# Kernel optimization log

Measured on AMD Instinct MI355X. Metric: run time of the kernel, lower is better.

## Reference

```python
import jax, jax.numpy as jnp
import numpy as np

H = 32        # num query heads
KVH = 8       # num kv heads
HD = 64       # head dim
G = H // KVH  # GQA group size
THETA = 10000.0


def _rope(x, pos):
    # x: [B, h, S, HD], pos: [B, S] int
    inv_freq = 1.0 / (THETA ** (jnp.arange(0, HD, 2, dtype=jnp.float32) / HD))  # [HD/2]
    freqs = pos.astype(jnp.float32)[:, :, None] * inv_freq[None, None, :]        # [B, S, HD/2]
    emb = jnp.concatenate([freqs, freqs], axis=-1)                               # [B, S, HD]
    cos = jnp.cos(emb)[:, None, :, :].astype(x.dtype)                            # [B, 1, S, HD]
    sin = jnp.sin(emb)[:, None, :, :].astype(x.dtype)
    x1, x2 = x[..., : HD // 2], x[..., HD // 2 :]
    rot = jnp.concatenate([-x2, x1], axis=-1)
    return x * cos + rot * sin


def setup_inputs() -> dict:
    key = jax.random.key(0)
    ks = jax.random.split(key, 8)
    B, S, D = 2, 2048, 2048
    s = 0.02
    hidden_states = jax.random.normal(ks[0], (B, S, D), dtype=jnp.float32)
    position_ids = jnp.broadcast_to(jnp.arange(S, dtype=jnp.int32)[None, :], (B, S))
    Wq = jax.random.normal(ks[1], (H * HD, D), dtype=jnp.float32) * s
    bq = jax.random.normal(ks[2], (H * HD,), dtype=jnp.float32) * s
    Wk = jax.random.normal(ks[3], (KVH * HD, D), dtype=jnp.float32) * s
    bk = jax.random.normal(ks[4], (KVH * HD,), dtype=jnp.float32) * s
    Wv = jax.random.normal(ks[5], (KVH * HD, D), dtype=jnp.float32) * s
    bv = jax.random.normal(ks[6], (KVH * HD,), dtype=jnp.float32) * s
    Wo = jax.random.normal(ks[7], (D, H * HD), dtype=jnp.float32) * s
    return dict(hidden_states=hidden_states, position_ids=position_ids,
                Wq=Wq, bq=bq, Wk=Wk, bk=bk, Wv=Wv, bv=bv, Wo=Wo)


def reference(hidden_states, position_ids, Wq, bq, Wk, bk, Wv, bv, Wo):
    B, S, D = hidden_states.shape
    scale = 1.0 / np.sqrt(HD)
    q = hidden_states @ Wq.T + bq  # [B, S, H*HD]
    k = hidden_states @ Wk.T + bk  # [B, S, KVH*HD]
    v = hidden_states @ Wv.T + bv
    q = q.reshape(B, S, H, HD).transpose(0, 2, 1, 3)      # [B, H, S, HD]
    k = k.reshape(B, S, KVH, HD).transpose(0, 2, 1, 3)    # [B, KVH, S, HD]
    v = v.reshape(B, S, KVH, HD).transpose(0, 2, 1, 3)
    q = _rope(q, position_ids)
    k = _rope(k, position_ids)
    # GQA: view q as [B, KVH, G, S, HD]; equivalent math to repeat_kv of k/v
    qg = q.reshape(B, KVH, G, S, HD)
    scores = jnp.einsum('bkgqd,bkld->bkgql', qg, k) * scale  # [B, KVH, G, S, S]
    # causal mask (past_seq_len = 0)
    causal = jnp.tril(jnp.ones((S, S), dtype=bool))
    scores = jnp.where(causal[None, None, None, :, :], scores, jnp.float32(-jnp.inf))
    attn = jax.nn.softmax(scores.astype(jnp.float32), axis=-1).astype(q.dtype)
    out = jnp.einsum('bkgql,bkld->bkgqd', attn, v)            # [B, KVH, G, S, HD]
    out = out.reshape(B, H, S, HD).transpose(0, 2, 1, 3).reshape(B, S, H * HD)
    return out @ Wo.T
```

## Files before the change

### kernel.cpp

```cpp
#include <hip/hip_runtime.h>
#include <hip/hip_bf16.h>

typedef unsigned short u16;
typedef __bf16 bf16x8 __attribute__((ext_vector_type(8)));
typedef float f32x4 __attribute__((ext_vector_type(4)));
typedef float f32x4v __attribute__((ext_vector_type(4)));
typedef unsigned short u16x4 __attribute__((ext_vector_type(4)));

__device__ __forceinline__ u16 f2bf(float f) {
  __bf16 h = (__bf16)f;
  return __builtin_bit_cast(unsigned short, h);
}

__device__ __forceinline__ int SW(int r, int c) {
  return (r << 6) + (c ^ ((r & 7) << 3));
}

#define GLOAD_LDS16(gp, lp) __builtin_amdgcn_global_load_lds( \
    (const __attribute__((address_space(1))) unsigned int*)(gp), \
    (__attribute__((address_space(3))) unsigned int*)(lp), 16, 0, 0)

__global__ void prep_all(const f32x4v* __restrict__ hs, u16x4* __restrict__ hsb,
                         const f32x4v* __restrict__ wq, const f32x4v* __restrict__ wk,
                         const f32x4v* __restrict__ wv, u16x4* __restrict__ wqkvb,
                         const f32x4v* __restrict__ wo, u16x4* __restrict__ wob,
                         const int* __restrict__ pos, float* __restrict__ cosT,
                         float* __restrict__ sinT, const float* __restrict__ bq,
                         const float* __restrict__ bk, const float* __restrict__ bv,
                         float* __restrict__ bc) {
  int i = blockIdx.x * 256 + threadIdx.x;
  if (i < 2097152) {
    f32x4v v = hs[i];
    u16x4 o; o.x = f2bf(v.x); o.y = f2bf(v.y); o.z = f2bf(v.z); o.w = f2bf(v.w);
    hsb[i] = o;
  } else if (i < 3670016) {
    int j = i - 2097152;
    f32x4v v = (j < 1048576) ? wq[j] : ((j < 1310720) ? wk[j - 1048576] : wv[j - 1310720]);
    u16x4 o; o.x = f2bf(v.x); o.y = f2bf(v.y); o.z = f2bf(v.z); o.w = f2bf(v.w);
    wqkvb[j] = o;
  } else if (i < 4718592) {
    int j = i - 3670016;
    f32x4v v = wo[j];
    u16x4 o; o.x = f2bf(v.x); o.y = f2bf(v.y); o.z = f2bf(v.z); o.w = f2bf(v.w);
    wob[j] = o;
  } else if (i < 4849664) {
    int j = i - 4718592;
    int bs = j >> 5, f = j & 31;
    float inv = exp2f(-(float)f * (13.287712379549449f / 32.f));
    float ang = (float)pos[bs] * inv;
    cosT[j] = cosf(ang);
    sinT[j] = sinf(ang);
  } else if (i < 4852736) {
    int j = i - 4849664;
    bc[j] = (j < 2048) ? bq[j] : ((j < 2560) ? bk[j - 2048] : bv[j - 2560]);
  }
}

template <int MODE>
__global__ __launch_bounds__(256, 2) void gemm_k(
    const u16* __restrict__ A, const u16* __restrict__ Bw, int K, int N,
    u16* __restrict__ qb, u16* __restrict__ kb, u16* __restrict__ vtb,
    const float* __restrict__ biasc, const float* __restrict__ cosT,
    const float* __restrict__ sinT, float* __restrict__ outf) {
  __shared__ u16 As[128 * 32];
  __shared__ u16 Bs[128 * 32];
  const int tid = threadIdx.x;
  const int lane = tid & 63, wid = tid >> 6;
  const int wr = wid >> 1, wc = wid & 1;
  const int col = lane & 15, rg = lane >> 4;
  const int tm = blockIdx.x, tn = blockIdx.y;
  const size_t K2 = (size_t)K * 2;

  const char* Ag = (const char*)(A + (size_t)tm * 128 * K) + (size_t)(tid >> 2) * K2 + (tid & 3) * 16;
  const char* Bg = (const char*)(Bw + (size_t)tn * 128 * K) + (size_t)(tid >> 2) * K2 + (tid & 3) * 16;
  char* AsW = (char*)As + wid * 1024;
  char* BsW = (char*)Bs + wid * 1024;

  f32x4 acc[4][4];
#pragma unroll
  for (int i = 0; i < 4; ++i)
#pragma unroll
    for (int j = 0; j < 4; ++j) acc[i][j] = (f32x4){0.f, 0.f, 0.f, 0.f};

  const u16* Ard = As + (wr * 64 + col) * 32 + rg * 8;
  const u16* Brd = Bs + (wc * 64 + col) * 32 + rg * 8;

  for (int k0 = 0; k0 < K; k0 += 32) {
    GLOAD_LDS16(Ag, AsW);
    GLOAD_LDS16(Ag + 64 * K2, AsW + 4096);
    GLOAD_LDS16(Bg, BsW);
    GLOAD_LDS16(Bg + 64 * K2, BsW + 4096);
    Ag += 64; Bg += 64;
    __syncthreads();
    bf16x8 af[4], bf[4];
#pragma unroll
    for (int i = 0; i < 4; ++i) af[i] = *(const bf16x8*)(Ard + i * 512);
#pragma unroll
    for (int j = 0; j < 4; ++j) bf[j] = *(const bf16x8*)(Brd + j * 512);
#pragma unroll
    for (int i = 0; i < 4; ++i)
#pragma unroll
      for (int j = 0; j < 4; ++j)
        acc[i][j] = __builtin_amdgcn_mfma_f32_16x16x32_bf16(af[i], bf[j], acc[i][j], 0, 0, 0);
    __syncthreads();
  }

  const int mg0 = tm * 128 + wr * 64;
  const int ng0 = tn * 128 + wc * 64;

  if (MODE == 1) {
#pragma unroll
    for (int i = 0; i < 4; ++i) {
      int m = mg0 + i * 16 + rg * 4;
#pragma unroll
      for (int j = 0; j < 4; ++j) {
        int n = ng0 + j * 16 + col;
#pragma unroll
        for (int r = 0; r < 4; ++r) outf[(size_t)(m + r) * N + n] = acc[i][j][r];
      }
    }
  } else {
    if (ng0 < 2048) {
      const float QS = 0.18033688011112042f;
      const int h = ng0 >> 6;
#pragma unroll
      for (int i = 0; i < 4; ++i)
#pragma unroll
        for (int r = 0; r < 4; ++r) {
          int m = mg0 + i * 16 + rg * 4 + r;
          int b = m >> 11, s = m & 2047;
          size_t base = ((size_t)(b * 32 + h) * 2048 + s) * 64;
#pragma unroll
          for (int j = 0; j < 2; ++j) {
            int d = j * 16 + col;
            float x1 = acc[i][j][r] + biasc[ng0 + d];
            float x2 = acc[i][j + 2][r] + biasc[ng0 + d + 32];
            float c = cosT[m * 32 + d], sn = sinT[m * 32 + d];
            qb[base + d]      = f2bf((x1 * c - x2 * sn) * QS);
            qb[base + d + 32] = f2bf((x2 * c + x1 * sn) * QS);
          }
        }
    } else if (ng0 < 2560) {
      const int hk = (ng0 - 2048) >> 6;
#pragma unroll
      for (int i = 0; i < 4; ++i)
#pragma unroll
        for (int r = 0; r < 4; ++r) {
          int m = mg0 + i * 16 + rg * 4 + r;
          int b = m >> 11, s = m & 2047;
          size_t base = ((size_t)(b * 8 + hk) * 2048 + s) * 64;
#pragma unroll
          for (int j = 0; j < 2; ++j) {
            int d = j * 16 + col;
            float x1 = acc[i][j][r] + biasc[ng0 + d];
            float x2 = acc[i][j + 2][r] + biasc[ng0 + d + 32];
            float c = cosT[m * 32 + d], sn = sinT[m * 32 + d];
            kb[base + d]      = f2bf(x1 * c - x2 * sn);
            kb[base + d + 32] = f2bf(x2 * c + x1 * sn);
          }
        }
    } else {
      const int hk = (ng0 - 2560) >> 6;
#pragma unroll
      for (int i = 0; i < 4; ++i)
#pragma unroll
        for (int r = 0; r < 4; ++r) {
          int m = mg0 + i * 16 + rg * 4 + r;
          int b = m >> 11, s = m & 2047;
#pragma unroll
          for (int j = 0; j < 4; ++j) {
            int d = j * 16 + col;
            float v = acc[i][j][r] + biasc[ng0 + d];
            vtb[((size_t)(b * 8 + hk) * 64 + d) * 2048 + s] = f2bf(v);
          }
        }
    }
  }
}

__global__ __launch_bounds__(256, 4) void attn_k(
    const u16* __restrict__ qb, const u16* __restrict__ kb,
    const u16* __restrict__ vtb, u16* __restrict__ attb) {
  __shared__ __align__(16) u16 Kl[2][2048];
  __shared__ __align__(16) u16 Vl[2][2048];
  __shared__ __align__(16) u16 Pl[4096];
  const int tid = threadIdx.x, lane = tid & 63, w = tid >> 6;
  const int col = lane & 15, rg = lane >> 4;

  const int bid = blockIdx.x;
  const int xcd = bid & 7, pos = bid >> 3;
  const int grp = xcd * 8 + (pos >> 4);
  const int s0 = pos & 15;
  const int strip = ((pos >> 5) & 1) ? (15 - s0) : s0;
  const int h = grp & 31, b = grp >> 5;
  const int qb0 = (15 - strip) * 128;
  const int hk = h >> 2;
  const int q0w = qb0 + w * 32;

  const u16* Qp = qb + ((size_t)(b * 32 + h) * 2048 + q0w + col) * 64 + rg * 8;
  bf16x8 qf[2][2];
#pragma unroll
  for (int g = 0; g < 2; ++g)
#pragma unroll
    for (int kf = 0; kf < 2; ++kf)
      qf[g][kf] = *(const bf16x8*)(Qp + g * 16 * 64 + kf * 32);

  f32x4 po[2][4];
  float l_part[2] = {0.f, 0.f};
#pragma unroll
  for (int g = 0; g < 2; ++g)
#pragma unroll
    for (int cf = 0; cf < 4; ++cf) po[g][cf] = (f32x4){0, 0, 0, 0};

  const u16* Kbase = kb + (size_t)(b * 8 + hk) * 2048 * 64;
  const u16* Vbase = vtb + (size_t)(b * 8 + hk) * 64 * 2048;
  const int srow = tid >> 3, c8 = (tid & 7) << 3;
  const int cs = c8 ^ ((srow & 7) << 3);
  const u16* Ksrc = Kbase + (size_t)srow * 64 + cs;
  const u16* Vsrc = Vbase + (size_t)(srow * 2 + (cs >> 5)) * 2048 + (cs & 31);
  char* Kdst0 = (char*)Kl + w * 1024;
  char* Vdst0 = (char*)Vl + w * 1024;

  const int nkv = (qb0 >> 5) + 4;
  const int rowmax = q0w + 31;

  GLOAD_LDS16(Ksrc, Kdst0);
  GLOAD_LDS16(Vsrc, Vdst0);
  __syncthreads();

  for (int it = 0; it < nkv; ++it) {
    const int kv0 = it * 32;
    const int buf = it & 1;
    if (it + 1 < nkv) {
      GLOAD_LDS16(Ksrc + (size_t)(it + 1) * 2048, Kdst0 + ((it + 1) & 1) * 4096);
      GLOAD_LDS16(Vsrc + (size_t)(it + 1) * 32, Vdst0 + ((it + 1) & 1) * 4096);
    }

    if (kv0 <= rowmax) {
      const u16* Kb = (const u16*)((const char*)Kl + buf * 4096);
      const u16* Vb = (const u16*)((const char*)Vl + buf * 4096);
      const bool diag = (kv0 + 32 > q0w);

#pragma unroll
      for (int cj = 0; cj < 2; ++cj) {
        const int krow = cj * 16 + col;
        bf16x8 k0f = *(const bf16x8*)&Kb[SW(krow, rg * 8)];
        bf16x8 k1f = *(const bf16x8*)&Kb[SW(krow, 32 + rg * 8)];
#pragma unroll
        for (int g = 0; g < 2; ++g) {
          f32x4 t = (f32x4){0, 0, 0, 0};
          t = __builtin_amdgcn_mfma_f32_16x16x32_bf16(k0f, qf[g][0], t, 0, 0, 0);
          t = __builtin_amdgcn_mfma_f32_16x16x32_bf16(k1f, qf[g][1], t, 0, 0, 0);
          const int q = q0w + g * 16 + col;
          if (diag) {
            const int kbase = kv0 + cj * 16 + rg * 4;
#pragma unroll
            for (int r = 0; r < 4; ++r)
              if (kbase + r > q) t[r] = -1e30f;
          }
          float p0 = __builtin_amdgcn_exp2f(t[0]);
          float p1 = __builtin_amdgcn_exp2f(t[1]);
          float p2 = __builtin_amdgcn_exp2f(t[2]);
          float p3 = __builtin_amdgcn_exp2f(t[3]);
          l_part[g] += (p0 + p1) + (p2 + p3);
          unsigned w0, w1;
          asm("v_cvt_pk_bf16_f32 %0, %1, %2" : "=v"(w0) : "v"(p0), "v"(p1));
          asm("v_cvt_pk_bf16_f32 %0, %1, %2" : "=v"(w1) : "v"(p2), "v"(p3));
          const int lq = w * 32 + g * 16 + col;
          const int prow = lq >> 1;
          const int pc = ((lq & 1) * 32 + cj * 16 + rg * 4) ^ ((prow & 7) << 3);
          *(uint2*)&Pl[prow * 64 + pc] = (uint2){w0, w1};
        }
      }

      __builtin_amdgcn_s_setprio(1);
      {
        bf16x8 pfr[2];
#pragma unroll
        for (int g = 0; g < 2; ++g) {
          const int lq = w * 32 + g * 16 + col;
          const int prow = lq >> 1;
          pfr[g] = *(const bf16x8*)&Pl[prow * 64 +
                     (((lq & 1) * 32 + rg * 8) ^ ((prow & 7) << 3))];
        }
#pragma unroll
        for (int cf = 0; cf < 4; ++cf) {
          const int d = cf * 16 + col;
          const int vrow = d >> 1;
          bf16x8 vf = *(const bf16x8*)&Vb[vrow * 64 +
                       (((d & 1) * 32 + rg * 8) ^ ((vrow & 7) << 3))];
          po[0][cf] = __builtin_amdgcn_mfma_f32_16x16x32_bf16(pfr[0], vf, po[0][cf], 0, 0, 0);
          po[1][cf] = __builtin_amdgcn_mfma_f32_16x16x32_bf16(pfr[1], vf, po[1][cf], 0, 0, 0);
        }
      }
      __builtin_amdgcn_s_setprio(0);
    }
    __syncthreads();
  }

#pragma unroll
  for (int g = 0; g < 2; ++g) {
    float l = l_part[g];
    l += __shfl_xor(l, 16);
    l += __shfl_xor(l, 32);
    l_part[g] = l;
  }
#pragma unroll
  for (int g = 0; g < 2; ++g)
#pragma unroll
    for (int r = 0; r < 4; ++r) {
      const float lq = __shfl(l_part[g], rg * 4 + r, 16);
      const float inv = 1.f / lq;
      const int qrow = q0w + g * 16 + rg * 4 + r;
      size_t base = ((size_t)b * 2048 + qrow) * 2048 + h * 64;
#pragma unroll
      for (int cf = 0; cf < 4; ++cf)
        attb[base + cf * 16 + col] = f2bf(po[g][cf][r] * inv);
    }
}

extern "C" void kernel_launch(void* const* d_in, const int* in_sizes, int n_in,
                              void* d_out, int out_size, void* d_ws, size_t ws_size,
                              hipStream_t stream) {
  const float* hs = (const float*)d_in[0];
  const int* pos = (const int*)d_in[1];
  const float* Wq = (const float*)d_in[2];
  const float* bq = (const float*)d_in[3];
  const float* Wk = (const float*)d_in[4];
  const float* bk = (const float*)d_in[5];
  const float* Wv = (const float*)d_in[6];
  const float* bv = (const float*)d_in[7];
  const float* Wo = (const float*)d_in[8];
  float* out = (float*)d_out;

  char* ws = (char*)d_ws;
  size_t off = 0;
  u16* hsb = (u16*)(ws + off);   off += (size_t)4096 * 2048 * 2;
  u16* wqkvb = (u16*)(ws + off); off += (size_t)3072 * 2048 * 2;
  u16* wob = (u16*)(ws + off);   off += (size_t)2048 * 2048 * 2;
  float* biasc = (float*)(ws + off); off += 3072 * 4;
  float* cosT = (float*)(ws + off);  off += (size_t)4096 * 32 * 4;
  float* sinT = (float*)(ws + off);  off += (size_t)4096 * 32 * 4;
  u16* qb = (u16*)(ws + off);    off += (size_t)2 * 32 * 2048 * 64 * 2;
  u16* kb = (u16*)(ws + off);    off += (size_t)2 * 8 * 2048 * 64 * 2;
  u16* vtb = (u16*)(ws + off);   off += (size_t)2 * 8 * 64 * 2048 * 2;
  u16* attb = (u16*)(ws + off);  off += (size_t)4096 * 2048 * 2;

  prep_all<<<18956, 256, 0, stream>>>((const f32x4v*)hs, (u16x4*)hsb,
                                      (const f32x4v*)Wq, (const f32x4v*)Wk,
                                      (const f32x4v*)Wv, (u16x4*)wqkvb,
                                      (const f32x4v*)Wo, (u16x4*)wob,
                                      pos, cosT, sinT, bq, bk, bv, biasc);

  gemm_k<0><<<dim3(32, 24), 256, 0, stream>>>(hsb, wqkvb, 2048, 3072,
                                              qb, kb, vtb, biasc, cosT, sinT, nullptr);
  attn_k<<<1024, 256, 0, stream>>>(qb, kb, vtb, attb);
  gemm_k<1><<<dim3(32, 16), 256, 0, stream>>>(attb, wob, 2048, 2048,
                                              nullptr, nullptr, nullptr, nullptr, nullptr, nullptr, out);
}
```

Measured before the change: 188.6 us.

## Replace GEMM with 256x256 double-buffered 8-wave kernel and permuted QK weight rows

```diff
diff --git a/kernel.cpp b/kernel.cpp
--- a/kernel.cpp
+++ b/kernel.cpp
@@ -12,6 +12,12 @@
   return __builtin_bit_cast(unsigned short, h);
 }
 
+__device__ __forceinline__ int permh(int ph) {
+  int blk = ph >> 4;
+  int pblk = (blk == 1) ? 2 : ((blk == 2) ? 1 : blk);
+  return (pblk << 4) | (ph & 15);
+}
+
 __device__ __forceinline__ int SW(int r, int c) {
   return (r << 6) + (c ^ ((r & 7) << 3));
 }
@@ -19,6 +25,9 @@
 #define GLOAD_LDS16(gp, lp) __builtin_amdgcn_global_load_lds( \
     (const __attribute__((address_space(1))) unsigned int*)(gp), \
     (__attribute__((address_space(3))) unsigned int*)(lp), 16, 0, 0)
+
+#define BAR() do { asm volatile("" ::: "memory"); __builtin_amdgcn_s_barrier(); asm volatile("" ::: "memory"); } while (0)
+#define VMCNT(n) asm volatile("s_waitcnt vmcnt(" #n ")" ::: "memory")
 
 __global__ void prep_all(const f32x4v* __restrict__ hs, u16x4* __restrict__ hsb,
                          const f32x4v* __restrict__ wq, const f32x4v* __restrict__ wk,
@@ -35,7 +44,18 @@
     hsb[i] = o;
   } else if (i < 3670016) {
     int j = i - 2097152;
-    f32x4v v = (j < 1048576) ? wq[j] : ((j < 1310720) ? wk[j - 1048576] : wv[j - 1310720]);
+    int row = j >> 9, c4 = j & 511;
+    f32x4v v;
+    if (row < 2048) {
+      int sr = (row & ~63) | permh(row & 63);
+      v = wq[(size_t)sr * 512 + c4];
+    } else if (row < 2560) {
+      int rk = row - 2048;
+      int sr = (rk & ~63) | permh(rk & 63);
+      v = wk[(size_t)sr * 512 + c4];
+    } else {
+      v = wv[(size_t)(row - 2560) * 512 + c4];
+    }
     u16x4 o; o.x = f2bf(v.x); o.y = f2bf(v.y); o.z = f2bf(v.z); o.w = f2bf(v.w);
     wqkvb[j] = o;
   } else if (i < 4718592) {
@@ -52,128 +72,216 @@
     sinT[j] = sinf(ang);
   } else if (i < 4852736) {
     int j = i - 4849664;
-    bc[j] = (j < 2048) ? bq[j] : ((j < 2560) ? bk[j - 2048] : bv[j - 2560]);
-  }
-}
+    float v;
+    if (j < 2048) {
+      v = bq[(j & ~63) | permh(j & 63)];
+    } else if (j < 2560) {
+      int jk = j - 2048;
+      v = bk[(jk & ~63) | permh(jk & 63)];
+    } else {
+      v = bv[j - 2560];
+    }
+    bc[j] = v;
+  }
+}
+
+#define STAGE8(op, kt, hh) { \
+    const u16* s_ = ((op) ? bS : aS) + (size_t)(hh) * 128 * K + (size_t)(kt) * 64; \
+    u16* d_ = lds + ((kt) & 1) * 32768 + (op) * 16384 + (hh) * 8192 + wid * 512; \
+    GLOAD_LDS16(s_, d_); \
+    GLOAD_LDS16(s_ + (size_t)64 * K, d_ + 4096); \
+  }
+
+#define LDA8(buf, qm) { \
+    const u16* p_ = lds + (buf) * 32768 + ((qm) * 128 + arow) * 64; \
+    _Pragma("unroll") \
+    for (int mf = 0; mf < 4; ++mf) { \
+      af[mf][0] = *(const bf16x8*)(p_ + mf * 1024 + koff0); \
+      af[mf][1] = *(const bf16x8*)(p_ + mf * 1024 + koff1); \
+    } }
+
+#define LDB8(buf, qn) { \
+    const u16* p_ = lds + (buf) * 32768 + 16384 + ((qn) * 128 + brow) * 64; \
+    _Pragma("unroll") \
+    for (int nf = 0; nf < 2; ++nf) { \
+      bfr[nf][0] = *(const bf16x8*)(p_ + nf * 1024 + koff0); \
+      bfr[nf][1] = *(const bf16x8*)(p_ + nf * 1024 + koff1); \
+    } }
+
+#define MM8(qm, qn) { \
+    __builtin_amdgcn_s_setprio(1); \
+    _Pragma("unroll") \
+    for (int mf = 0; mf < 4; ++mf) \
+      _Pragma("unroll") \
+      for (int nf = 0; nf < 2; ++nf) { \
+        acc[(qm) * 4 + mf][(qn) * 2 + nf] = __builtin_amdgcn_mfma_f32_16x16x32_bf16( \
+            af[mf][0], bfr[nf][0], acc[(qm) * 4 + mf][(qn) * 2 + nf], 0, 0, 0); \
+        acc[(qm) * 4 + mf][(qn) * 2 + nf] = __builtin_amdgcn_mfma_f32_16x16x32_bf16( \
+            af[mf][1], bfr[nf][1], acc[(qm) * 4 + mf][(qn) * 2 + nf], 0, 0, 0); \
+      } \
+    __builtin_amdgcn_s_setprio(0); }
 
 template <int MODE>
-__global__ __launch_bounds__(256, 2) void gemm_k(
-    const u16* __restrict__ A, const u16* __restrict__ Bw, int K, int N,
+__global__ __launch_bounds__(512, 2) void gemm8(
+    const u16* __restrict__ A, const u16* __restrict__ Bw, const int K, const int N,
     u16* __restrict__ qb, u16* __restrict__ kb, u16* __restrict__ vtb,
     const float* __restrict__ biasc, const float* __restrict__ cosT,
     const float* __restrict__ sinT, float* __restrict__ outf) {
-  __shared__ u16 As[128 * 32];
-  __shared__ u16 Bs[128 * 32];
+  __shared__ u16 lds[65536];
   const int tid = threadIdx.x;
   const int lane = tid & 63, wid = tid >> 6;
-  const int wr = wid >> 1, wc = wid & 1;
+  const int wr = wid >> 2, wc = wid & 3;
   const int col = lane & 15, rg = lane >> 4;
   const int tm = blockIdx.x, tn = blockIdx.y;
-  const size_t K2 = (size_t)K * 2;
-
-  const char* Ag = (const char*)(A + (size_t)tm * 128 * K) + (size_t)(tid >> 2) * K2 + (tid & 3) * 16;
-  const char* Bg = (const char*)(Bw + (size_t)tn * 128 * K) + (size_t)(tid >> 2) * K2 + (tid & 3) * 16;
-  char* AsW = (char*)As + wid * 1024;
-  char* BsW = (char*)Bs + wid * 1024;
-
-  f32x4 acc[4][4];
-#pragma unroll
-  for (int i = 0; i < 4; ++i)
+
+  const int srow = tid >> 3;
+  const int scol = ((tid & 7) ^ (srow & 7)) * 8;
+  const u16* aS = A + ((size_t)tm * 256 + srow) * K + scol;
+  const u16* bS = Bw + ((size_t)tn * 256 + srow) * K + scol;
+
+  const int koff0 = (rg ^ (col & 7)) * 8;
+  const int koff1 = ((4 + rg) ^ (col & 7)) * 8;
+  const int arow = wr * 64 + col;
+  const int brow = wc * 32 + col;
+
+  f32x4 acc[8][4];
+#pragma unroll
+  for (int i = 0; i < 8; ++i)
 #pragma unroll
     for (int j = 0; j < 4; ++j) acc[i][j] = (f32x4){0.f, 0.f, 0.f, 0.f};
-
-  const u16* Ard = As + (wr * 64 + col) * 32 + rg * 8;
-  const u16* Brd = Bs + (wc * 64 + col) * 32 + rg * 8;
-
-  for (int k0 = 0; k0 < K; k0 += 32) {
-    GLOAD_LDS16(Ag, AsW);
-    GLOAD_LDS16(Ag + 64 * K2, AsW + 4096);
-    GLOAD_LDS16(Bg, BsW);
-    GLOAD_LDS16(Bg + 64 * K2, BsW + 4096);
-    Ag += 64; Bg += 64;
-    __syncthreads();
-    bf16x8 af[4], bf[4];
-#pragma unroll
-    for (int i = 0; i < 4; ++i) af[i] = *(const bf16x8*)(Ard + i * 512);
-#pragma unroll
-    for (int j = 0; j < 4; ++j) bf[j] = *(const bf16x8*)(Brd + j * 512);
-#pragma unroll
-    for (int i = 0; i < 4; ++i)
-#pragma unroll
-      for (int j = 0; j < 4; ++j)
-        acc[i][j] = __builtin_amdgcn_mfma_f32_16x16x32_bf16(af[i], bf[j], acc[i][j], 0, 0, 0);
-    __syncthreads();
-  }
-
-  const int mg0 = tm * 128 + wr * 64;
-  const int ng0 = tn * 128 + wc * 64;
+  bf16x8 af[4][2], bfr[2][2];
+
+  const int ITERS = K >> 7;
+
+  STAGE8(0, 0, 0); STAGE8(0, 0, 1);
+  STAGE8(1, 0, 0); STAGE8(1, 0, 1);
+  STAGE8(0, 1, 0); STAGE8(1, 1, 1); STAGE8(0, 1, 1);
+  VMCNT(6);
+  BAR();
+
+#pragma unroll 1
+  for (int it = 0; it < ITERS; ++it) {
+    const int t0 = it * 2;
+    const bool more = (it + 1 < ITERS);
+    LDA8(0, 0); LDB8(0, 0);
+    STAGE8(1, t0 + 1, 0);
+    BAR(); MM8(0, 0); BAR();
+    LDB8(0, 1);
+    if (more) STAGE8(0, t0 + 2, 0);
+    BAR(); MM8(0, 1); BAR();
+    LDA8(0, 1);
+    if (more) STAGE8(1, t0 + 2, 1);
+    BAR(); MM8(1, 1); BAR();
+    LDB8(0, 0);
+    if (more) STAGE8(0, t0 + 2, 1);
+    BAR(); MM8(1, 0);
+    if (more) { VMCNT(6); } else { VMCNT(0); }
+    BAR();
+    LDA8(1, 0); LDB8(1, 0);
+    if (more) STAGE8(1, t0 + 2, 0);
+    BAR(); MM8(0, 0); BAR();
+    LDB8(1, 1);
+    if (more) STAGE8(0, t0 + 3, 0);
+    BAR(); MM8(0, 1); BAR();
+    LDA8(1, 1);
+    if (more) STAGE8(1, t0 + 3, 1);
+    BAR(); MM8(1, 1); BAR();
+    LDB8(1, 0);
+    if (more) STAGE8(0, t0 + 3, 1);
+    BAR(); MM8(1, 0);
+    if (more) VMCNT(6);
+    BAR();
+  }
 
   if (MODE == 1) {
 #pragma unroll
-    for (int i = 0; i < 4; ++i) {
-      int m = mg0 + i * 16 + rg * 4;
-#pragma unroll
-      for (int j = 0; j < 4; ++j) {
-        int n = ng0 + j * 16 + col;
-#pragma unroll
-        for (int r = 0; r < 4; ++r) outf[(size_t)(m + r) * N + n] = acc[i][j][r];
+    for (int qm = 0; qm < 2; ++qm)
+#pragma unroll
+      for (int mf = 0; mf < 4; ++mf) {
+        const int mbase = tm * 256 + qm * 128 + wr * 64 + mf * 16 + rg * 4;
+#pragma unroll
+        for (int qn = 0; qn < 2; ++qn)
+#pragma unroll
+          for (int nf = 0; nf < 2; ++nf) {
+            const int n = tn * 256 + qn * 128 + wc * 32 + nf * 16 + col;
+#pragma unroll
+            for (int r = 0; r < 4; ++r)
+              outf[(size_t)(mbase + r) * N + n] = acc[qm * 4 + mf][qn * 2 + nf][r];
+          }
       }
-    }
   } else {
-    if (ng0 < 2048) {
+    if (tn < 8) {
       const float QS = 0.18033688011112042f;
-      const int h = ng0 >> 6;
-#pragma unroll
-      for (int i = 0; i < 4; ++i)
-#pragma unroll
-        for (int r = 0; r < 4; ++r) {
-          int m = mg0 + i * 16 + rg * 4 + r;
-          int b = m >> 11, s = m & 2047;
-          size_t base = ((size_t)(b * 32 + h) * 2048 + s) * 64;
-#pragma unroll
-          for (int j = 0; j < 2; ++j) {
-            int d = j * 16 + col;
-            float x1 = acc[i][j][r] + biasc[ng0 + d];
-            float x2 = acc[i][j + 2][r] + biasc[ng0 + d + 32];
-            float c = cosT[m * 32 + d], sn = sinT[m * 32 + d];
-            qb[base + d]      = f2bf((x1 * c - x2 * sn) * QS);
-            qb[base + d + 32] = f2bf((x2 * c + x1 * sn) * QS);
-          }
+#pragma unroll
+      for (int qm = 0; qm < 2; ++qm)
+#pragma unroll
+        for (int qn = 0; qn < 2; ++qn) {
+          const int h = tn * 4 + qn * 2 + (wc >> 1);
+          const int c32 = wc & 1;
+          const int n0 = tn * 256 + qn * 128 + wc * 32 + col;
+          const float b1 = biasc[n0], b2 = biasc[n0 + 16];
+          const int f = c32 * 16 + col;
+          const int ph0 = c32 * 32 + col;
+#pragma unroll
+          for (int mf = 0; mf < 4; ++mf)
+#pragma unroll
+            for (int r = 0; r < 4; ++r) {
+              const int m = tm * 256 + qm * 128 + wr * 64 + mf * 16 + rg * 4 + r;
+              const int b = m >> 11, s = m & 2047;
+              const size_t base = ((size_t)(b * 32 + h) * 2048 + s) * 64;
+              float x1 = acc[qm * 4 + mf][qn * 2 + 0][r] + b1;
+              float x2 = acc[qm * 4 + mf][qn * 2 + 1][r] + b2;
+              float c = cosT[m * 32 + f], sn = sinT[m * 32 + f];
+              qb[base + ph0]      = f2bf((x1 * c - x2 * sn) * QS);
+              qb[base + ph0 + 16] = f2bf((x2 * c + x1 * sn) * QS);
+            }
         }
-    } else if (ng0 < 2560) {
-      const int hk = (ng0 - 2048) >> 6;
-#pragma unroll
-      for (int i = 0; i < 4; ++i)
-#pragma unroll
-        for (int r = 0; r < 4; ++r) {
-          int m = mg0 + i * 16 + rg * 4 + r;
-          int b = m >> 11, s = m & 2047;
-          size_t base = ((size_t)(b * 8 + hk) * 2048 + s) * 64;
-#pragma unroll
-          for (int j = 0; j < 2; ++j) {
-            int d = j * 16 + col;
-            float x1 = acc[i][j][r] + biasc[ng0 + d];
-            float x2 = acc[i][j + 2][r] + biasc[ng0 + d + 32];
-            float c = cosT[m * 32 + d], sn = sinT[m * 32 + d];
-            kb[base + d]      = f2bf(x1 * c - x2 * sn);
-            kb[base + d + 32] = f2bf(x2 * c + x1 * sn);
-          }
+    } else if (tn < 10) {
+#pragma unroll
+      for (int qm = 0; qm < 2; ++qm)
+#pragma unroll
+        for (int qn = 0; qn < 2; ++qn) {
+          const int hk = (tn - 8) * 4 + qn * 2 + (wc >> 1);
+          const int c32 = wc & 1;
+          const int n0 = tn * 256 + qn * 128 + wc * 32 + col;
+          const float b1 = biasc[n0], b2 = biasc[n0 + 16];
+          const int f = c32 * 16 + col;
+          const int ph0 = c32 * 32 + col;
+#pragma unroll
+          for (int mf = 0; mf < 4; ++mf)
+#pragma unroll
+            for (int r = 0; r < 4; ++r) {
+              const int m = tm * 256 + qm * 128 + wr * 64 + mf * 16 + rg * 4 + r;
+              const int b = m >> 11, s = m & 2047;
+              const size_t base = ((size_t)(b * 8 + hk) * 2048 + s) * 64;
+              float x1 = acc[qm * 4 + mf][qn * 2 + 0][r] + b1;
+              float x2 = acc[qm * 4 + mf][qn * 2 + 1][r] + b2;
+              float c = cosT[m * 32 + f], sn = sinT[m * 32 + f];
+              kb[base + ph0]      = f2bf(x1 * c - x2 * sn);
+              kb[base + ph0 + 16] = f2bf(x2 * c + x1 * sn);
+            }
         }
     } else {
-      const int hk = (ng0 - 2560) >> 6;
-#pragma unroll
-      for (int i = 0; i < 4; ++i)
-#pragma unroll
-        for (int r = 0; r < 4; ++r) {
-          int m = mg0 + i * 16 + rg * 4 + r;
-          int b = m >> 11, s = m & 2047;
-#pragma unroll
-          for (int j = 0; j < 4; ++j) {
-            int d = j * 16 + col;
-            float v = acc[i][j][r] + biasc[ng0 + d];
-            vtb[((size_t)(b * 8 + hk) * 64 + d) * 2048 + s] = f2bf(v);
+#pragma unroll
+      for (int qm = 0; qm < 2; ++qm)
+#pragma unroll
+        for (int qn = 0; qn < 2; ++qn)
+#pragma unroll
+          for (int nf = 0; nf < 2; ++nf) {
+            const int n = tn * 256 + qn * 128 + wc * 32 + nf * 16 + col;
+            const int hk = (n - 2560) >> 6;
+            const int d = (n - 2560) & 63;
+            const float bvv = biasc[n];
+#pragma unroll
+            for (int mf = 0; mf < 4; ++mf)
+#pragma unroll
+              for (int r = 0; r < 4; ++r) {
+                const int m = tm * 256 + qm * 128 + wr * 64 + mf * 16 + rg * 4 + r;
+                const int b = m >> 11, s = m & 2047;
+                vtb[((size_t)(b * 8 + hk) * 64 + d) * 2048 + s] =
+                    f2bf(acc[qm * 4 + mf][qn * 2 + nf][r] + bvv);
+              }
           }
-        }
     }
   }
 }
@@ -352,9 +460,10 @@
                                       (const f32x4v*)Wo, (u16x4*)wob,
                                       pos, cosT, sinT, bq, bk, bv, biasc);
 
-  gemm_k<0><<<dim3(32, 24), 256, 0, stream>>>(hsb, wqkvb, 2048, 3072,
-                                              qb, kb, vtb, biasc, cosT, sinT, nullptr);
+  gemm8<0><<<dim3(16, 12), 512, 0, stream>>>(hsb, wqkvb, 2048, 3072,
+                                             qb, kb, vtb, biasc, cosT, sinT, nullptr);
   attn_k<<<1024, 256, 0, stream>>>(qb, kb, vtb, attb);
-  gemm_k<1><<<dim3(32, 16), 256, 0, stream>>>(attb, wob, 2048, 2048,
-                                              nullptr, nullptr, nullptr, nullptr, nullptr, nullptr, out);
-}
+  gemm8<1><<<dim3(16, 8), 512, 0, stream>>>(attb, wob, 2048, 2048,
+                                            nullptr, nullptr, nullptr, nullptr,
+                                            nullptr, nullptr, out);
+}
```

After: 200.9 us. 6.5% more time.
